# Kernel optimization log

Hardware: AMD Instinct MI355X
Metric: run time of the kernel (lower is better)

Reference implementation:

```python
import jax, jax.numpy as jnp
import numpy as np

D_MODEL = 1024
NUM_HEADS = 16
HEAD_DIM = D_MODEL // NUM_HEADS
D_FF = 4096
LN_EPS = 1e-6  # flax nnx.LayerNorm default


def setup_inputs() -> dict:
    key = jax.random.key(0)
    ks = jax.random.split(key, 13)
    s_in = 1.0 / np.sqrt(D_MODEL)
    s_ff = 1.0 / np.sqrt(D_FF)
    return {
        "x": jax.random.normal(ks[0], (2, 2048, D_MODEL), dtype=jnp.float32),
        "Wq": jax.random.normal(ks[1], (D_MODEL, D_MODEL), jnp.float32) * s_in,
        "bq": jnp.zeros((D_MODEL,), jnp.float32),
        "Wk": jax.random.normal(ks[2], (D_MODEL, D_MODEL), jnp.float32) * s_in,
        "bk": jnp.zeros((D_MODEL,), jnp.float32),
        "Wv": jax.random.normal(ks[3], (D_MODEL, D_MODEL), jnp.float32) * s_in,
        "bv": jnp.zeros((D_MODEL,), jnp.float32),
        "Wo": jax.random.normal(ks[4], (D_MODEL, D_MODEL), jnp.float32) * s_in,
        "bo": jnp.zeros((D_MODEL,), jnp.float32),
        "W1": jax.random.normal(ks[5], (D_MODEL, D_FF), jnp.float32) * s_in,
        "b1": jnp.zeros((D_FF,), jnp.float32),
        "W2": jax.random.normal(ks[6], (D_FF, D_MODEL), jnp.float32) * s_ff,
        "b2": jnp.zeros((D_MODEL,), jnp.float32),
        "ln1_scale": jnp.ones((D_MODEL,), jnp.float32),
        "ln1_bias": jnp.zeros((D_MODEL,), jnp.float32),
        "ln2_scale": jnp.ones((D_MODEL,), jnp.float32),
        "ln2_bias": jnp.zeros((D_MODEL,), jnp.float32),
    }


def layer_norm(x, scale, bias):
    mu = jnp.mean(x, axis=-1, keepdims=True)
    var = jnp.mean(jnp.square(x - mu), axis=-1, keepdims=True)
    return (x - mu) * jax.lax.rsqrt(var + LN_EPS) * scale + bias


def reference(x, Wq, bq, Wk, bk, Wv, bv, Wo, bo, W1, b1, W2, b2,
              ln1_scale, ln1_bias, ln2_scale, ln2_bias):
    B, S, _ = x.shape
    h = layer_norm(x, ln1_scale, ln1_bias)
    # project and split heads: [B, H, S, Dh]
    q = (h @ Wq + bq).reshape(B, S, NUM_HEADS, HEAD_DIM).transpose(0, 2, 1, 3)
    k = (h @ Wk + bk).reshape(B, S, NUM_HEADS, HEAD_DIM).transpose(0, 2, 1, 3)
    v = (h @ Wv + bv).reshape(B, S, NUM_HEADS, HEAD_DIM).transpose(0, 2, 1, 3)
    scores = jnp.einsum("bhqd,bhkd->bhqk", q, k) / jnp.sqrt(jnp.float32(HEAD_DIM))
    attn = jax.nn.softmax(scores, axis=-1)
    out = jnp.einsum("bhqk,bhkd->bhqd", attn, v)
    out = out.transpose(0, 2, 1, 3).reshape(B, S, D_MODEL)
    x = x + out @ Wo + bo
    h2 = layer_norm(x, ln2_scale, ln2_bias)
    ff = jax.nn.relu(h2 @ W1 + b1) @ W2 + b2
    return x + ff
```

## Files before the change

kernel.cpp:

```cpp
#include <hip/hip_runtime.h>

typedef unsigned short ushort_t;
typedef __attribute__((ext_vector_type(8))) __bf16 bf16x8;
typedef __attribute__((ext_vector_type(8))) unsigned short ushort8v;
typedef __attribute__((ext_vector_type(4))) float floatx4;

__device__ inline float b2f(ushort_t u) {
    union { unsigned int i; float f; } c; c.i = ((unsigned int)u) << 16; return c.f;
}
__device__ inline ushort_t f2b(float f) {
    union { float f; unsigned int i; } c; c.f = f;
    unsigned int i = c.i;
    unsigned int r = (i + 0x7FFFu + ((i >> 16) & 1u)) >> 16;
    return (ushort_t)r;
}
__device__ inline bf16x8 as_bf16x8(ushort8v u) { return __builtin_bit_cast(bf16x8, u); }

__device__ inline void load_lds16(const ushort_t* g, ushort_t* l) {
    __builtin_amdgcn_global_load_lds(
        (const __attribute__((address_space(1))) void*)g,
        (__attribute__((address_space(3))) void*)l, 16, 0, 0);
}

__global__ __launch_bounds__(256) void concat3_kernel(
    const float* __restrict__ a, const float* __restrict__ b,
    const float* __restrict__ c, float* __restrict__ o) {
    int t = blockIdx.x * 256 + threadIdx.x;
    if (t < 3072)
        o[t] = t < 1024 ? a[t] : (t < 2048 ? b[t - 1024] : c[t - 2048]);
}

__global__ __launch_bounds__(256) void copy_f32_kernel(
    const float* __restrict__ src, float* __restrict__ dst) {
    size_t i = ((size_t)blockIdx.x * 256 + threadIdx.x) * 4;
    *(float4*)(dst + i) = *(const float4*)(src + i);
}

__global__ __launch_bounds__(256) void transpose_all_kernel(
    const float* __restrict__ Wq, const float* __restrict__ Wk,
    const float* __restrict__ Wv, const float* __restrict__ Wo,
    const float* __restrict__ W1, const float* __restrict__ W2,
    ushort_t* __restrict__ dq, ushort_t* __restrict__ dk,
    ushort_t* __restrict__ dv, ushort_t* __restrict__ do_,
    ushort_t* __restrict__ d1, ushort_t* __restrict__ d2) {
    int t = blockIdx.x;
    const float* src; ushort_t* dst; int R, ld, tcx, tcy;
    if (t < 4096) {
        int id = t >> 10, u = t & 1023;
        tcx = u & 31; tcy = u >> 5; R = 1024; ld = 1024;
        src = id == 0 ? Wq : id == 1 ? Wk : id == 2 ? Wv : Wo;
        dst = id == 0 ? dq : id == 1 ? dk : id == 2 ? dv : do_;
    } else if (t < 8192) {
        int u = t - 4096;
        tcx = u & 127; tcy = u >> 7; R = 1024; ld = 4096;
        src = W1; dst = d1;
    } else {
        int u = t - 8192;
        tcx = u & 31; tcy = u >> 5; R = 4096; ld = 1024;
        src = W2; dst = d2;
    }
    __shared__ float tile[32][33];
    int tx = threadIdx.x, ty = threadIdx.y;
    int r0 = tcy * 32, c0 = tcx * 32;
#pragma unroll
    for (int i = 0; i < 32; i += 8)
        tile[ty + i][tx] = src[(size_t)(r0 + ty + i) * ld + c0 + tx];
    __syncthreads();
#pragma unroll
    for (int i = 0; i < 32; i += 8)
        dst[(size_t)(c0 + ty + i) * R + r0 + tx] = f2b(tile[tx][ty + i]);
}

__global__ __launch_bounds__(256) void transpose_v_kernel(
    const ushort_t* __restrict__ qkv, ushort_t* __restrict__ vt) {
    __shared__ ushort_t tile[32][33];
    int tx = threadIdx.x, ty = threadIdx.y;
    int s0 = blockIdx.x * 32, d0 = blockIdx.y * 32;
    int bh = blockIdx.z, b = bh >> 4, h = bh & 15;
    const ushort_t* src = qkv + (size_t)b * 2048 * 3072 + 2048 + h * 64;
    ushort_t* dst = vt + (size_t)bh * 64 * 2048;
#pragma unroll
    for (int i = 0; i < 32; i += 8)
        tile[ty + i][tx] = src[(size_t)(s0 + ty + i) * 3072 + d0 + tx];
    __syncthreads();
#pragma unroll
    for (int i = 0; i < 32; i += 8)
        dst[(size_t)(d0 + ty + i) * 2048 + s0 + tx] = tile[tx][ty + i];
}

__device__ inline float wave_sum(float s) {
#pragma unroll
    for (int o = 32; o > 0; o >>= 1) s += __shfl_xor(s, o);
    return s;
}

__global__ __launch_bounds__(256) void ln_f32_kernel(
    const float* __restrict__ x, const float* __restrict__ sc,
    const float* __restrict__ bi, ushort_t* __restrict__ out) {
    int row = blockIdx.x, t = threadIdx.x;
    const float* xr = x + (size_t)row * 1024;
    float4 u = *(const float4*)(xr + t * 4);
    float v0 = u.x, v1 = u.y, v2 = u.z, v3 = u.w;
    __shared__ float sm[8];
    int wv = t >> 6, lane = t & 63;
    float s = wave_sum(v0 + v1 + v2 + v3);
    if (lane == 0) sm[wv] = s;
    __syncthreads();
    float mean = (sm[0] + sm[1] + sm[2] + sm[3]) * (1.0f / 1024.0f);
    float d0 = v0 - mean, d1 = v1 - mean, d2 = v2 - mean, d3 = v3 - mean;
    float q = wave_sum(d0 * d0 + d1 * d1 + d2 * d2 + d3 * d3);
    if (lane == 0) sm[4 + wv] = q;
    __syncthreads();
    float var = (sm[4] + sm[5] + sm[6] + sm[7]) * (1.0f / 1024.0f);
    float rn = rsqrtf(var + 1e-6f);
    float4 us = *(const float4*)(sc + t * 4);
    float4 ub = *(const float4*)(bi + t * 4);
    ushort4 o;
    o.x = f2b(d0 * rn * us.x + ub.x);
    o.y = f2b(d1 * rn * us.y + ub.y);
    o.z = f2b(d2 * rn * us.z + ub.z);
    o.w = f2b(d3 * rn * us.w + ub.w);
    *(ushort4*)(out + (size_t)row * 1024 + t * 4) = o;
}

__global__ __launch_bounds__(256) void gemm_bt_kernel(
    const ushort_t* __restrict__ A, const ushort_t* __restrict__ Bt,
    const float* __restrict__ bias, const float* __restrict__ resf,
    ushort_t* __restrict__ Cb, float* __restrict__ Cf,
    int M, int N, int K, int ldb, int op) {
    __shared__ __align__(16) ushort_t As[128 * 64];
    __shared__ __align__(16) ushort_t Bs[128 * 64];
    int tid = threadIdx.x;
    int m0 = blockIdx.y * 128, n0 = blockIdx.x * 128;
    int wv = tid >> 6, lane = tid & 63;
    int wr = wv & 1, wc = wv >> 1;
    int mo = wr * 64, no = wc * 64;
    int quad = lane >> 4, l16 = lane & 15;
    int k8 = quad * 8;

    floatx4 acc[4][4] = {};

    for (int k0 = 0; k0 < K; k0 += 64) {
#pragma unroll
        for (int c = 0; c < 4; ++c) {
            int e = c * 2048 + tid * 8;
            int r = e >> 6, kk = e & 63;
            int wbase = c * 2048 + wv * 512;
            load_lds16(A + (size_t)(m0 + r) * K + k0 + kk, As + wbase);
            load_lds16(Bt + (size_t)(n0 + r) * ldb + k0 + kk, Bs + wbase);
        }
        __syncthreads();
#pragma unroll
        for (int h = 0; h < 2; ++h) {
            bf16x8 af[4], bfr[4];
#pragma unroll
            for (int i = 0; i < 4; ++i) {
                af[i]  = as_bf16x8(*(const ushort8v*)(As + (mo + i * 16 + l16) * 64 + h * 32 + k8));
                bfr[i] = as_bf16x8(*(const ushort8v*)(Bs + (no + i * 16 + l16) * 64 + h * 32 + k8));
            }
#pragma unroll
            for (int mi = 0; mi < 4; ++mi)
#pragma unroll
                for (int ni = 0; ni < 4; ++ni)
                    acc[mi][ni] = __builtin_amdgcn_mfma_f32_16x16x32_bf16(
                        af[mi], bfr[ni], acc[mi][ni], 0, 0, 0);
        }
        __syncthreads();
    }

#pragma unroll
    for (int mi = 0; mi < 4; ++mi) {
#pragma unroll
        for (int r = 0; r < 4; ++r) {
            int row = m0 + mo + mi * 16 + quad * 4 + r;
            size_t rowoff = (size_t)row * N;
#pragma unroll
            for (int ni = 0; ni < 4; ++ni) {
                int col = n0 + no + ni * 16 + l16;
                float val = acc[mi][ni][r];
                if (op != 3) val += bias[col];
                if (op == 1) val = fmaxf(val, 0.0f);
                if (op >= 2) {
                    val += resf[rowoff + col];
                    Cf[rowoff + col] = val;
                } else {
                    Cb[rowoff + col] = f2b(val);
                }
            }
        }
    }
}

__global__ __launch_bounds__(256) void gemm_bt_atomic_kernel(
    const ushort_t* __restrict__ A, const ushort_t* __restrict__ Bt,
    const float* __restrict__ bias, float* __restrict__ Cf,
    int M, int N, int lda, int ldb, int Kc) {
    __shared__ __align__(16) ushort_t As[128 * 64];
    __shared__ __align__(16) ushort_t Bs[128 * 64];
    int tid = threadIdx.x;
    int m0 = blockIdx.y * 128, n0 = blockIdx.x * 128;
    int kbase = blockIdx.z * Kc;
    int wv = tid >> 6, lane = tid & 63;
    int wr = wv & 1, wc = wv >> 1;
    int mo = wr * 64, no = wc * 64;
    int quad = lane >> 4, l16 = lane & 15;
    int k8 = quad * 8;

    floatx4 acc[4][4] = {};

    for (int k0 = kbase; k0 < kbase + Kc; k0 += 64) {
#pragma unroll
        for (int c = 0; c < 4; ++c) {
            int e = c * 2048 + tid * 8;
            int r = e >> 6, kk = e & 63;
            int wbase = c * 2048 + wv * 512;
            load_lds16(A + (size_t)(m0 + r) * lda + k0 + kk, As + wbase);
            load_lds16(Bt + (size_t)(n0 + r) * ldb + k0 + kk, Bs + wbase);
        }
        __syncthreads();
#pragma unroll
        for (int h = 0; h < 2; ++h) {
            bf16x8 af[4], bfr[4];
#pragma unroll
            for (int i = 0; i < 4; ++i) {
                af[i]  = as_bf16x8(*(const ushort8v*)(As + (mo + i * 16 + l16) * 64 + h * 32 + k8));
                bfr[i] = as_bf16x8(*(const ushort8v*)(Bs + (no + i * 16 + l16) * 64 + h * 32 + k8));
            }
#pragma unroll
            for (int mi = 0; mi < 4; ++mi)
#pragma unroll
                for (int ni = 0; ni < 4; ++ni)
                    acc[mi][ni] = __builtin_amdgcn_mfma_f32_16x16x32_bf16(
                        af[mi], bfr[ni], acc[mi][ni], 0, 0, 0);
        }
        __syncthreads();
    }

    bool addb = (blockIdx.z == 0) && (bias != nullptr);
#pragma unroll
    for (int mi = 0; mi < 4; ++mi) {
#pragma unroll
        for (int r = 0; r < 4; ++r) {
            int row = m0 + mo + mi * 16 + quad * 4 + r;
            size_t rowoff = (size_t)row * N;
#pragma unroll
            for (int ni = 0; ni < 4; ++ni) {
                int col = n0 + no + ni * 16 + l16;
                float val = acc[mi][ni][r];
                if (addb) val += bias[col];
                unsafeAtomicAdd(&Cf[rowoff + col], val);
            }
        }
    }
}

__global__ __launch_bounds__(256) void attn_kernel(
    const ushort_t* __restrict__ qkv, const ushort_t* __restrict__ vt,
    ushort_t* __restrict__ om) {
    const int LDQ = 3072, LDO = 1024;
    int bh = blockIdx.y;
    int b = bh >> 4, h = bh & 15;
    size_t qbase = (size_t)b * 2048 * LDQ + h * 64;
    size_t kbase = qbase + 1024;
    const ushort_t* vtp = vt + (size_t)bh * 64 * 2048;
    int q0 = blockIdx.x * 128;
    int tid = threadIdx.x, wv = tid >> 6, lane = tid & 63;
    int quad = lane >> 4, l16 = lane & 15;
    int k8 = quad * 8;

    __shared__ __align__(16) ushort_t Ks[64 * 72];
    __shared__ __align__(16) ushort_t Vs[64 * 72];
    __shared__ __align__(16) ushort_t Ps[4 * 32 * 76];
    ushort_t* ps = Ps + wv * 32 * 76;

    int sr0 = tid >> 3, scc0 = (tid & 7) * 8;
    int sr1 = sr0 + 32;

    bf16x8 qf[2][2];
#pragma unroll
    for (int mt = 0; mt < 2; ++mt) {
        const ushort_t* qptr = qkv + qbase + (size_t)(q0 + wv * 32 + mt * 16 + l16) * LDQ;
        qf[mt][0] = as_bf16x8(*(const ushort8v*)(qptr + k8));
        qf[mt][1] = as_bf16x8(*(const ushort8v*)(qptr + 32 + k8));
    }

    bf16x8 ones;
#pragma unroll
    for (int j = 0; j < 8; ++j) ones[j] = (__bf16)1.0f;

    floatx4 Oacc[2][4] = {};
    floatx4 lsum[2] = {};

    ushort8v kreg0, kreg1, vreg0, vreg1;
    kreg0 = *(const ushort8v*)(qkv + kbase + (size_t)sr0 * LDQ + scc0);
    kreg1 = *(const ushort8v*)(qkv + kbase + (size_t)sr1 * LDQ + scc0);
    vreg0 = *(const ushort8v*)(vtp + (size_t)sr0 * 2048 + scc0);
    vreg1 = *(const ushort8v*)(vtp + (size_t)sr1 * 2048 + scc0);

    for (int kb = 0; kb < 2048; kb += 64) {
        __syncthreads();
        *(ushort8v*)(Ks + sr0 * 72 + scc0) = kreg0;
        *(ushort8v*)(Ks + sr1 * 72 + scc0) = kreg1;
        *(ushort8v*)(Vs + sr0 * 72 + scc0) = vreg0;
        *(ushort8v*)(Vs + sr1 * 72 + scc0) = vreg1;
        __syncthreads();

        int nkb = (kb + 64 < 2048) ? kb + 64 : 0;
        kreg0 = *(const ushort8v*)(qkv + kbase + (size_t)(nkb + sr0) * LDQ + scc0);
        kreg1 = *(const ushort8v*)(qkv + kbase + (size_t)(nkb + sr1) * LDQ + scc0);
        vreg0 = *(const ushort8v*)(vtp + (size_t)sr0 * 2048 + nkb + scc0);
        vreg1 = *(const ushort8v*)(vtp + (size_t)sr1 * 2048 + nkb + scc0);

        bf16x8 kf[4][2];
#pragma unroll
        for (int kt = 0; kt < 4; ++kt)
#pragma unroll
            for (int ds = 0; ds < 2; ++ds)
                kf[kt][ds] = as_bf16x8(
                    *(const ushort8v*)(Ks + (kt * 16 + l16) * 72 + ds * 32 + k8));

        floatx4 sc[2][4];
#pragma unroll
        for (int mt = 0; mt < 2; ++mt)
#pragma unroll
            for (int kt = 0; kt < 4; ++kt) {
                floatx4 s = {0.0f, 0.0f, 0.0f, 0.0f};
                s = __builtin_amdgcn_mfma_f32_16x16x32_bf16(kf[kt][0], qf[mt][0], s, 0, 0, 0);
                s = __builtin_amdgcn_mfma_f32_16x16x32_bf16(kf[kt][1], qf[mt][1], s, 0, 0, 0);
                sc[mt][kt] = s;
            }

#pragma unroll
        for (int mt = 0; mt < 2; ++mt)
#pragma unroll
            for (int kt = 0; kt < 4; ++kt) {
                ushort4 pk;
                pk.x = f2b(__expf(sc[mt][kt][0] * 0.125f));
                pk.y = f2b(__expf(sc[mt][kt][1] * 0.125f));
                pk.z = f2b(__expf(sc[mt][kt][2] * 0.125f));
                pk.w = f2b(__expf(sc[mt][kt][3] * 0.125f));
                *(ushort4*)(ps + (mt * 16 + l16) * 76 + kt * 16 + quad * 4) = pk;
            }

        bf16x8 vf[4][2];
#pragma unroll
        for (int dt = 0; dt < 4; ++dt)
#pragma unroll
            for (int ks = 0; ks < 2; ++ks)
                vf[dt][ks] = as_bf16x8(
                    *(const ushort8v*)(Vs + (dt * 16 + l16) * 72 + ks * 32 + k8));
#pragma unroll
        for (int mt = 0; mt < 2; ++mt) {
            bf16x8 pf0 = as_bf16x8(*(const ushort8v*)(ps + (mt * 16 + l16) * 76 + k8));
            bf16x8 pf1 = as_bf16x8(*(const ushort8v*)(ps + (mt * 16 + l16) * 76 + 32 + k8));
#pragma unroll
            for (int dt = 0; dt < 4; ++dt) {
                Oacc[mt][dt] = __builtin_amdgcn_mfma_f32_16x16x32_bf16(pf0, vf[dt][0], Oacc[mt][dt], 0, 0, 0);
                Oacc[mt][dt] = __builtin_amdgcn_mfma_f32_16x16x32_bf16(pf1, vf[dt][1], Oacc[mt][dt], 0, 0, 0);
            }
            lsum[mt] = __builtin_amdgcn_mfma_f32_16x16x32_bf16(pf0, ones, lsum[mt], 0, 0, 0);
            lsum[mt] = __builtin_amdgcn_mfma_f32_16x16x32_bf16(pf1, ones, lsum[mt], 0, 0, 0);
        }
    }

#pragma unroll
    for (int mt = 0; mt < 2; ++mt)
#pragma unroll
        for (int r = 0; r < 4; ++r) {
            float inv = 1.0f / lsum[mt][r];
            size_t rowoff = (size_t)(b * 2048 + q0 + wv * 32 + mt * 16 + quad * 4 + r) * LDO + h * 64;
#pragma unroll
            for (int dt = 0; dt < 4; ++dt)
                om[rowoff + dt * 16 + l16] = f2b(Oacc[mt][dt][r] * inv);
        }
}

extern "C" void kernel_launch(void* const* d_in, const int* in_sizes, int n_in,
                              void* d_out, int out_size, void* d_ws, size_t ws_size,
                              hipStream_t stream) {
    const float* x    = (const float*)d_in[0];
    const float* Wq   = (const float*)d_in[1];
    const float* bq   = (const float*)d_in[2];
    const float* Wk   = (const float*)d_in[3];
    const float* bk   = (const float*)d_in[4];
    const float* Wv   = (const float*)d_in[5];
    const float* bv   = (const float*)d_in[6];
    const float* Wo   = (const float*)d_in[7];
    const float* bo   = (const float*)d_in[8];
    const float* W1   = (const float*)d_in[9];
    const float* b1   = (const float*)d_in[10];
    const float* W2   = (const float*)d_in[11];
    const float* b2   = (const float*)d_in[12];
    const float* ln1s = (const float*)d_in[13];
    const float* ln1b = (const float*)d_in[14];
    const float* ln2s = (const float*)d_in[15];
    const float* ln2b = (const float*)d_in[16];
    float*    outf = (float*)d_out;
    ushort_t* ws   = (ushort_t*)d_ws;

    const size_t M1 = 1048576;
    ushort_t* qkvT    = ws;
    ushort_t* WoT     = ws + 3 * M1;
    ushort_t* W1T     = ws + 4 * M1;
    ushort_t* W2T     = ws + 8 * M1;
    ushort_t* h       = ws + 12 * M1;
    ushort_t* attnout = ws + 12 * M1;
    ushort_t* qkv     = ws + 16 * M1;
    ushort_t* h2      = ws;
    ushort_t* ffbuf   = ws + 12 * M1;
    float*    bqkv    = (float*)d_out;
    ushort_t* vtbuf   = (ushort_t*)d_out;

    dim3 tb(32, 8);

    concat3_kernel<<<12, 256, 0, stream>>>(bq, bk, bv, bqkv);
    transpose_all_kernel<<<12288, tb, 0, stream>>>(
        Wq, Wk, Wv, Wo, W1, W2,
        qkvT, qkvT + M1, qkvT + 2 * M1, WoT, W1T, W2T);

    ln_f32_kernel<<<4096, 256, 0, stream>>>(x, ln1s, ln1b, h);

    gemm_bt_kernel<<<dim3(24, 32), 256, 0, stream>>>(
        h, qkvT, bqkv, nullptr, qkv, nullptr, 4096, 3072, 1024, 1024, 0);

    transpose_v_kernel<<<dim3(64, 2, 32), tb, 0, stream>>>(qkv, vtbuf);

    attn_kernel<<<dim3(16, 32), 256, 0, stream>>>(qkv, vtbuf, attnout);

    copy_f32_kernel<<<4096, 256, 0, stream>>>(x, outf);
    gemm_bt_atomic_kernel<<<dim3(8, 32, 4), 256, 0, stream>>>(
        attnout, WoT, bo, outf, 4096, 1024, 1024, 1024, 256);

    ln_f32_kernel<<<4096, 256, 0, stream>>>(outf, ln2s, ln2b, h2);

    gemm_bt_kernel<<<dim3(32, 32), 256, 0, stream>>>(
        h2, W1T, b1, nullptr, ffbuf, nullptr, 4096, 4096, 1024, 1024, 1);

    gemm_bt_atomic_kernel<<<dim3(8, 32, 2), 256, 0, stream>>>(
        ffbuf, W2T, b2, outf, 4096, 1024, 4096, 4096, 2048);
}
```

Measured before the change: 508.1 us.

## Double-buffer GEMM LDS tiles, use native bf16 conversion, raise W2 split-K

```diff
diff --git a/kernel.cpp b/kernel.cpp
--- a/kernel.cpp
+++ b/kernel.cpp
@@ -2,6 +2,7 @@
 
 typedef unsigned short ushort_t;
 typedef __attribute__((ext_vector_type(8))) __bf16 bf16x8;
+typedef __attribute__((ext_vector_type(4))) __bf16 bf16x4;
 typedef __attribute__((ext_vector_type(8))) unsigned short ushort8v;
 typedef __attribute__((ext_vector_type(4))) float floatx4;
 
@@ -128,8 +129,8 @@
     const float* __restrict__ bias, const float* __restrict__ resf,
     ushort_t* __restrict__ Cb, float* __restrict__ Cf,
     int M, int N, int K, int ldb, int op) {
-    __shared__ __align__(16) ushort_t As[128 * 64];
-    __shared__ __align__(16) ushort_t Bs[128 * 64];
+    __shared__ __align__(16) ushort_t As[2][128 * 32];
+    __shared__ __align__(16) ushort_t Bs[2][128 * 32];
     int tid = threadIdx.x;
     int m0 = blockIdx.y * 128, n0 = blockIdx.x * 128;
     int wv = tid >> 6, lane = tid & 63;
@@ -140,32 +141,40 @@
 
     floatx4 acc[4][4] = {};
 
-    for (int k0 = 0; k0 < K; k0 += 64) {
-#pragma unroll
-        for (int c = 0; c < 4; ++c) {
-            int e = c * 2048 + tid * 8;
-            int r = e >> 6, kk = e & 63;
-            int wbase = c * 2048 + wv * 512;
-            load_lds16(A + (size_t)(m0 + r) * K + k0 + kk, As + wbase);
-            load_lds16(Bt + (size_t)(n0 + r) * ldb + k0 + kk, Bs + wbase);
-        }
+    int e0 = tid * 8, e1 = 2048 + tid * 8;
+    int r0 = e0 >> 5, kk0 = e0 & 31;
+    int r1 = e1 >> 5, kk1 = e1 & 31;
+    int wb0 = wv * 512, wb1 = 2048 + wv * 512;
+
+    load_lds16(A + (size_t)(m0 + r0) * K + kk0, As[0] + wb0);
+    load_lds16(Bt + (size_t)(n0 + r0) * ldb + kk0, Bs[0] + wb0);
+    load_lds16(A + (size_t)(m0 + r1) * K + kk1, As[0] + wb1);
+    load_lds16(Bt + (size_t)(n0 + r1) * ldb + kk1, Bs[0] + wb1);
+
+    int buf = 0;
+    for (int k0 = 0; k0 < K; k0 += 32) {
         __syncthreads();
-#pragma unroll
-        for (int h = 0; h < 2; ++h) {
-            bf16x8 af[4], bfr[4];
-#pragma unroll
-            for (int i = 0; i < 4; ++i) {
-                af[i]  = as_bf16x8(*(const ushort8v*)(As + (mo + i * 16 + l16) * 64 + h * 32 + k8));
-                bfr[i] = as_bf16x8(*(const ushort8v*)(Bs + (no + i * 16 + l16) * 64 + h * 32 + k8));
-            }
-#pragma unroll
-            for (int mi = 0; mi < 4; ++mi)
-#pragma unroll
-                for (int ni = 0; ni < 4; ++ni)
-                    acc[mi][ni] = __builtin_amdgcn_mfma_f32_16x16x32_bf16(
-                        af[mi], bfr[ni], acc[mi][ni], 0, 0, 0);
-        }
-        __syncthreads();
+        int nk = k0 + 32;
+        if (nk < K) {
+            int nb = buf ^ 1;
+            load_lds16(A + (size_t)(m0 + r0) * K + nk + kk0, As[nb] + wb0);
+            load_lds16(Bt + (size_t)(n0 + r0) * ldb + nk + kk0, Bs[nb] + wb0);
+            load_lds16(A + (size_t)(m0 + r1) * K + nk + kk1, As[nb] + wb1);
+            load_lds16(Bt + (size_t)(n0 + r1) * ldb + nk + kk1, Bs[nb] + wb1);
+        }
+        bf16x8 af[4], bfr[4];
+#pragma unroll
+        for (int i = 0; i < 4; ++i) {
+            af[i]  = as_bf16x8(*(const ushort8v*)(As[buf] + (mo + i * 16 + l16) * 32 + k8));
+            bfr[i] = as_bf16x8(*(const ushort8v*)(Bs[buf] + (no + i * 16 + l16) * 32 + k8));
+        }
+#pragma unroll
+        for (int mi = 0; mi < 4; ++mi)
+#pragma unroll
+            for (int ni = 0; ni < 4; ++ni)
+                acc[mi][ni] = __builtin_amdgcn_mfma_f32_16x16x32_bf16(
+                    af[mi], bfr[ni], acc[mi][ni], 0, 0, 0);
+        buf ^= 1;
     }
 
 #pragma unroll
@@ -195,8 +204,8 @@
     const ushort_t* __restrict__ A, const ushort_t* __restrict__ Bt,
     const float* __restrict__ bias, float* __restrict__ Cf,
     int M, int N, int lda, int ldb, int Kc) {
-    __shared__ __align__(16) ushort_t As[128 * 64];
-    __shared__ __align__(16) ushort_t Bs[128 * 64];
+    __shared__ __align__(16) ushort_t As[2][128 * 32];
+    __shared__ __align__(16) ushort_t Bs[2][128 * 32];
     int tid = threadIdx.x;
     int m0 = blockIdx.y * 128, n0 = blockIdx.x * 128;
     int kbase = blockIdx.z * Kc;
@@ -208,32 +217,40 @@
 
     floatx4 acc[4][4] = {};
 
-    for (int k0 = kbase; k0 < kbase + Kc; k0 += 64) {
-#pragma unroll
-        for (int c = 0; c < 4; ++c) {
-            int e = c * 2048 + tid * 8;
-            int r = e >> 6, kk = e & 63;
-            int wbase = c * 2048 + wv * 512;
-            load_lds16(A + (size_t)(m0 + r) * lda + k0 + kk, As + wbase);
-            load_lds16(Bt + (size_t)(n0 + r) * ldb + k0 + kk, Bs + wbase);
-        }
+    int e0 = tid * 8, e1 = 2048 + tid * 8;
+    int r0 = e0 >> 5, kk0 = e0 & 31;
+    int r1 = e1 >> 5, kk1 = e1 & 31;
+    int wb0 = wv * 512, wb1 = 2048 + wv * 512;
+
+    load_lds16(A + (size_t)(m0 + r0) * lda + kbase + kk0, As[0] + wb0);
+    load_lds16(Bt + (size_t)(n0 + r0) * ldb + kbase + kk0, Bs[0] + wb0);
+    load_lds16(A + (size_t)(m0 + r1) * lda + kbase + kk1, As[0] + wb1);
+    load_lds16(Bt + (size_t)(n0 + r1) * ldb + kbase + kk1, Bs[0] + wb1);
+
+    int buf = 0;
+    for (int k0 = kbase; k0 < kbase + Kc; k0 += 32) {
         __syncthreads();
-#pragma unroll
-        for (int h = 0; h < 2; ++h) {
-            bf16x8 af[4], bfr[4];
-#pragma unroll
-            for (int i = 0; i < 4; ++i) {
-                af[i]  = as_bf16x8(*(const ushort8v*)(As + (mo + i * 16 + l16) * 64 + h * 32 + k8));
-                bfr[i] = as_bf16x8(*(const ushort8v*)(Bs + (no + i * 16 + l16) * 64 + h * 32 + k8));
-            }
-#pragma unroll
-            for (int mi = 0; mi < 4; ++mi)
-#pragma unroll
-                for (int ni = 0; ni < 4; ++ni)
-                    acc[mi][ni] = __builtin_amdgcn_mfma_f32_16x16x32_bf16(
-                        af[mi], bfr[ni], acc[mi][ni], 0, 0, 0);
-        }
-        __syncthreads();
+        int nk = k0 + 32;
+        if (nk < kbase + Kc) {
+            int nb = buf ^ 1;
+            load_lds16(A + (size_t)(m0 + r0) * lda + nk + kk0, As[nb] + wb0);
+            load_lds16(Bt + (size_t)(n0 + r0) * ldb + nk + kk0, Bs[nb] + wb0);
+            load_lds16(A + (size_t)(m0 + r1) * lda + nk + kk1, As[nb] + wb1);
+            load_lds16(Bt + (size_t)(n0 + r1) * ldb + nk + kk1, Bs[nb] + wb1);
+        }
+        bf16x8 af[4], bfr[4];
+#pragma unroll
+        for (int i = 0; i < 4; ++i) {
+            af[i]  = as_bf16x8(*(const ushort8v*)(As[buf] + (mo + i * 16 + l16) * 32 + k8));
+            bfr[i] = as_bf16x8(*(const ushort8v*)(Bs[buf] + (no + i * 16 + l16) * 32 + k8));
+        }
+#pragma unroll
+        for (int mi = 0; mi < 4; ++mi)
+#pragma unroll
+            for (int ni = 0; ni < 4; ++ni)
+                acc[mi][ni] = __builtin_amdgcn_mfma_f32_16x16x32_bf16(
+                    af[mi], bfr[ni], acc[mi][ni], 0, 0, 0);
+        buf ^= 1;
     }
 
     bool addb = (blockIdx.z == 0) && (bias != nullptr);
@@ -334,12 +351,12 @@
         for (int mt = 0; mt < 2; ++mt)
 #pragma unroll
             for (int kt = 0; kt < 4; ++kt) {
-                ushort4 pk;
-                pk.x = f2b(__expf(sc[mt][kt][0] * 0.125f));
-                pk.y = f2b(__expf(sc[mt][kt][1] * 0.125f));
-                pk.z = f2b(__expf(sc[mt][kt][2] * 0.125f));
-                pk.w = f2b(__expf(sc[mt][kt][3] * 0.125f));
-                *(ushort4*)(ps + (mt * 16 + l16) * 76 + kt * 16 + quad * 4) = pk;
+                bf16x4 pb;
+                pb[0] = (__bf16)__expf(sc[mt][kt][0] * 0.125f);
+                pb[1] = (__bf16)__expf(sc[mt][kt][1] * 0.125f);
+                pb[2] = (__bf16)__expf(sc[mt][kt][2] * 0.125f);
+                pb[3] = (__bf16)__expf(sc[mt][kt][3] * 0.125f);
+                *(bf16x4*)(ps + (mt * 16 + l16) * 76 + kt * 16 + quad * 4) = pb;
             }
 
         bf16x8 vf[4][2];
@@ -436,6 +453,6 @@
     gemm_bt_kernel<<<dim3(32, 32), 256, 0, stream>>>(
         h2, W1T, b1, nullptr, ffbuf, nullptr, 4096, 4096, 1024, 1024, 1);
 
-    gemm_bt_atomic_kernel<<<dim3(8, 32, 2), 256, 0, stream>>>(
-        ffbuf, W2T, b2, outf, 4096, 1024, 4096, 4096, 2048);
-}
+    gemm_bt_atomic_kernel<<<dim3(8, 32, 4), 256, 0, stream>>>(
+        ffbuf, W2T, b2, outf, 4096, 1024, 4096, 4096, 1024);
+}
```

New measurement: 494.4 us. 1.03x faster.
